# Performance work log

Hardware: AMD Instinct MI355X
Metric: run time of the kernel (lower is better)

Reference implementation:

```python
import jax, jax.numpy as jnp
import numpy as np

B, L, D = 4, 2048, 256
H, HD = 8, 64
MAX_LEN = 2048


def setup_inputs() -> dict:
    key = jax.random.key(0)
    ks = jax.random.split(key, 5)
    x = jax.random.normal(ks[0], (B, L, D), dtype=jnp.float32)
    glorot_q = (2.0 / (D + H * HD)) ** 0.5
    Wq = jax.random.normal(ks[1], (D, H * HD), dtype=jnp.float32) * glorot_q
    Wk = jax.random.normal(ks[2], (D, H * HD), dtype=jnp.float32) * glorot_q
    bq = jnp.zeros((H, 1, 1, HD), dtype=jnp.float32)
    bk = jnp.zeros((H, 1, 1, HD), dtype=jnp.float32)
    prior_mean = jax.random.uniform(ks[3], (H,), dtype=jnp.float32, minval=-1.0, maxval=1.0)
    log_prior_std = jnp.full((H,), np.log(0.4), dtype=jnp.float32)
    return {"x": x, "Wq": Wq, "bq": bq, "Wk": Wk, "bk": bk,
            "prior_mean": prior_mean, "log_prior_std": log_prior_std,
            "max_length": MAX_LEN}


def _gaussian(x, mean, std):
    return 1.0 / std / jnp.sqrt(2.0 * 3.1415926) * jnp.exp(-0.5 * (x - mean) ** 2 / std ** 2)


def reference(x, Wq, bq, Wk, bk, prior_mean, log_prior_std, max_length):
    b, l, d = x.shape
    h, hd = bq.shape[0], bq.shape[-1]
    # normalized signed distance matrix [l, l]
    r = jnp.arange(l, dtype=jnp.float32)
    dist = (r[None, :] - r[:, None]) / float(max_length)
    # projections -> [h, b, l, hd] (split heads along last dim, heads leading)
    q = (x @ Wq).reshape(b, l, h, hd).transpose(2, 0, 1, 3) + bq
    k = (x @ Wk).reshape(b, l, h, hd).transpose(2, 0, 1, 3) + bk
    # gaussian positional prior per head [h, l, l]
    prior = _gaussian(dist[None, :, :], prior_mean[:, None, None],
                      jnp.exp(log_prior_std)[:, None, None])
    # scaled QK^T * prior -> softmax over keys
    scores = jnp.einsum('hbqd,hbkd->hbqk', q, k) * (float(hd) ** -0.5)
    att = jax.nn.softmax(scores * prior[:, None, :, :], axis=-1)
    # distance-weighted reduction instead of V-matmul: [h, b, l] -> [b, l, h]
    distance = jnp.einsum('hbqk,qk->hbq', att, dist)
    return distance.transpose(1, 2, 0)
```

## Files before the change

### kernel.cpp

```cpp
#include <hip/hip_runtime.h>
#include <math.h>


#define B_  4
#define L_  2048
#define D_  256
#define H_  8
#define HD_ 64

typedef unsigned int u32;
typedef unsigned short u16;
typedef short bf16x8 __attribute__((ext_vector_type(8)));
typedef float f32x4  __attribute__((ext_vector_type(4)));

union U16x8 { u16 u[8]; bf16x8 v; uint4 q; };

__device__ __forceinline__ u16 bf16rne(float v) {
    u32 u = __float_as_uint(v);
    return (u16)((u + 0x7fffu + ((u >> 16) & 1u)) >> 16);
}
__device__ __forceinline__ float bf2f(u16 h) { return __uint_as_float(((u32)h) << 16); }

__global__ __launch_bounds__(256, 4) void proj_kernel(
    const float* __restrict__ x,
    const float* __restrict__ Wq, const float* __restrict__ bq,
    const float* __restrict__ Wk, const float* __restrict__ bk,
    u16* __restrict__ Qhi, u16* __restrict__ Qlo,
    u16* __restrict__ Khi, u16* __restrict__ Klo)
{
    __shared__ __align__(16) u16 Bs[2][64][40];

    const int z = blockIdx.z;
    const float* W    = z ? Wk : Wq;
    const float* bias = z ? bk : bq;
    u16* Ohi = z ? Khi : Qhi;
    u16* Olo = z ? Klo : Qlo;

    const int t = threadIdx.x, w = t >> 6, l = t & 63;
    const int kc = l & 15, lhi = l >> 4;
    const int m0 = blockIdx.x * 128 + w * 32;
    const int h  = blockIdx.y;

    const float* xp0 = x + (size_t)(m0 + kc) * D_;
    const float* xp1 = x + (size_t)(m0 + 16 + kc) * D_;

    f32x4 acc[2][4];
    #pragma unroll
    for (int mf = 0; mf < 2; ++mf)
        #pragma unroll
        for (int nf = 0; nf < 4; ++nf) acc[mf][nf] = (f32x4){0.f, 0.f, 0.f, 0.f};

    for (int ks = 0; ks < 8; ++ks) {
        __syncthreads();
        #pragma unroll
        for (int j = 0; j < 2; ++j) {
            const int fid = t + j * 256;
            const int kr = fid >> 4, c4 = fid & 15;
            float4 v = *(const float4*)&W[(size_t)(ks*32 + kr) * 512 + h*64 + c4*4];
            float vv[4] = {v.x, v.y, v.z, v.w};
            #pragma unroll
            for (int e = 0; e < 4; ++e) {
                const int n = c4*4 + e;
                const u16 hi = bf16rne(vv[e]);
                Bs[0][n][kr] = hi;
                Bs[1][n][kr] = bf16rne(vv[e] - bf2f(hi));
            }
        }
        __syncthreads();

        U16x8 ah[2], al[2];
        #pragma unroll
        for (int mf = 0; mf < 2; ++mf) {
            const float* xp = mf ? xp1 : xp0;
            float4 a = *(const float4*)(xp + ks*32 + lhi*8);
            float4 b = *(const float4*)(xp + ks*32 + lhi*8 + 4);
            float vv[8] = {a.x, a.y, a.z, a.w, b.x, b.y, b.z, b.w};
            #pragma unroll
            for (int e = 0; e < 8; ++e) {
                const u16 hi = bf16rne(vv[e]);
                ah[mf].u[e] = hi;
                al[mf].u[e] = bf16rne(vv[e] - bf2f(hi));
            }
        }

        #pragma unroll
        for (int nf = 0; nf < 4; ++nf) {
            const bf16x8 bh = *(const bf16x8*)&Bs[0][nf*16 + kc][lhi*8];
            const bf16x8 bl = *(const bf16x8*)&Bs[1][nf*16 + kc][lhi*8];
            #pragma unroll
            for (int mf = 0; mf < 2; ++mf) {
                acc[mf][nf] = __builtin_amdgcn_mfma_f32_16x16x32_bf16(ah[mf].v, bh, acc[mf][nf], 0, 0, 0);
                acc[mf][nf] = __builtin_amdgcn_mfma_f32_16x16x32_bf16(ah[mf].v, bl, acc[mf][nf], 0, 0, 0);
                acc[mf][nf] = __builtin_amdgcn_mfma_f32_16x16x32_bf16(al[mf].v, bh, acc[mf][nf], 0, 0, 0);
            }
        }
    }

    #pragma unroll
    for (int mf = 0; mf < 2; ++mf)
        #pragma unroll
        for (int nf = 0; nf < 4; ++nf) {
            const float bv = bias[h * 64 + nf*16 + kc];
            #pragma unroll
            for (int r = 0; r < 4; ++r) {
                const float v = acc[mf][nf][r] + bv;
                const u16 hi = bf16rne(v);
                const u16 lo = bf16rne(v - bf2f(hi));
                const int m = m0 + mf*16 + lhi*4 + r;
                const int bb = m >> 11, ll = m & (L_ - 1);
                const size_t o = (((size_t)h * B_ + bb) * L_ + ll) * HD_ + nf*16 + kc;
                Ohi[o] = hi; Olo[o] = lo;
            }
        }
}

__global__ __launch_bounds__(512, 4) void attn_kernel(
    const u16* __restrict__ Qhi, const u16* __restrict__ Qlo,
    const u16* __restrict__ Khi, const u16* __restrict__ Klo,
    const float* __restrict__ prior_mean, const float* __restrict__ log_prior_std,
    const int* __restrict__ max_len, float* __restrict__ out)
{
    __shared__ __align__(16) u16 kls[2][64 * 64];
    __shared__ float2 Ptab[2176];

    const int t = threadIdx.x, w = t >> 6, l = t & 63;
    const int kc = l & 15, lhi = l >> 4;
    const int q0 = blockIdx.x * 128;
    const int hb = blockIdx.y, h = hb >> 2, b = hb & 3;
    const int qw = q0 + w * 16;

    const float iml = 1.0f / (float)(*max_len);
    const float mu  = prior_mean[h];
    const float sg  = __expf(log_prior_std[h]);
    const float isg = 1.0f / sg;
    const float coef = 0.125f / (sg * 2.5066282746310002f) * 1.44269504089f;
    for (int i = t; i < 2175; i += 512) {
        const float dist = (float)(i - q0 - 127) * iml;
        const float tt = (dist - mu) * isg;
        Ptab[i] = make_float2(coef * __expf(-0.5f * tt * tt), dist);
    }

    bf16x8 qh[2], ql2[2];
    #pragma unroll
    for (int dh = 0; dh < 2; ++dh) {
        const size_t qo = ((size_t)hb * L_ + qw + kc) * HD_ + dh*32 + lhi*8;
        qh[dh]  = *(const bf16x8*)&Qhi[qo];
        ql2[dh] = *(const bf16x8*)&Qlo[qo];
    }

    const float2* pbase = &Ptab[lhi*4 + 127 - w*16 - kc];

    const int spl = t >> 8;
    const int srow = (t & 255) >> 2;
    const int sq = t & 3;
    const int sr7 = srow & 7;
    const u16* Kg = (spl ? Klo : Khi) + ((size_t)hb * L_ + srow) * HD_ + sq * 16;
    u16* lds_row = &kls[spl][srow * 64];

    const int sl0 = lhi ^ (l & 7);
    const int sl1 = (4 + lhi) ^ (l & 7);

    float lv = 0.f, wv = 0.f;

    for (int kt = 0; kt < 32; ++kt) {
        __syncthreads();
        {
            const u16* src = Kg + (size_t)kt * 64 * HD_;
            const uint4 g0 = *(const uint4*)src;
            const uint4 g1 = *(const uint4*)(src + 8);
            const int p0 = (sq*2)     ^ sr7;
            const int p1 = (sq*2 + 1) ^ sr7;
            *(uint4*)&lds_row[p0 * 8] = g0;
            *(uint4*)&lds_row[p1 * 8] = g1;
        }
        __syncthreads();

        f32x4 acc[4];
        #pragma unroll
        for (int kf = 0; kf < 4; ++kf) acc[kf] = (f32x4){0.f, 0.f, 0.f, 0.f};

        #pragma unroll
        for (int kf = 0; kf < 4; ++kf) {
            const int rbase = (kf*16 + kc) * 64;
            const bf16x8 ah0 = *(const bf16x8*)&kls[0][rbase + sl0*8];
            const bf16x8 ah1 = *(const bf16x8*)&kls[0][rbase + sl1*8];
            const bf16x8 al0 = *(const bf16x8*)&kls[1][rbase + sl0*8];
            const bf16x8 al1 = *(const bf16x8*)&kls[1][rbase + sl1*8];
            acc[kf] = __builtin_amdgcn_mfma_f32_16x16x32_bf16(ah0, qh[0],  acc[kf], 0, 0, 0);
            acc[kf] = __builtin_amdgcn_mfma_f32_16x16x32_bf16(ah1, qh[1],  acc[kf], 0, 0, 0);
            acc[kf] = __builtin_amdgcn_mfma_f32_16x16x32_bf16(ah0, ql2[0], acc[kf], 0, 0, 0);
            acc[kf] = __builtin_amdgcn_mfma_f32_16x16x32_bf16(ah1, ql2[1], acc[kf], 0, 0, 0);
            acc[kf] = __builtin_amdgcn_mfma_f32_16x16x32_bf16(al0, qh[0],  acc[kf], 0, 0, 0);
            acc[kf] = __builtin_amdgcn_mfma_f32_16x16x32_bf16(al1, qh[1],  acc[kf], 0, 0, 0);
        }

        const float2* pp = pbase + kt * 64;
        #pragma unroll
        for (int kf = 0; kf < 4; ++kf)
            #pragma unroll
            for (int r = 0; r < 4; ++r) {
                const float2 pd = pp[kf*16 + r];
                const float e = exp2f(acc[kf][r] * pd.x);
                lv += e;
                wv = fmaf(e, pd.y, wv);
            }
    }

    lv += __shfl_xor(lv, 16); wv += __shfl_xor(wv, 16);
    lv += __shfl_xor(lv, 32); wv += __shfl_xor(wv, 32);
    if (lhi == 0) {
        const int q = qw + kc;
        out[((size_t)(b * L_ + q)) * H_ + h] = wv / lv;
    }
}

extern "C" void kernel_launch(void* const* d_in, const int* in_sizes, int n_in,
                              void* d_out, int out_size, void* d_ws, size_t ws_size,
                              hipStream_t stream)
{
    const float* x   = (const float*)d_in[0];
    const float* Wq  = (const float*)d_in[1];
    const float* bq  = (const float*)d_in[2];
    const float* Wk  = (const float*)d_in[3];
    const float* bk  = (const float*)d_in[4];
    const float* pm  = (const float*)d_in[5];
    const float* lps = (const float*)d_in[6];
    const int*   mlp = (const int*)d_in[7];
    float* out = (float*)d_out;

    u16* Qhi = (u16*)d_ws;
    u16* Qlo = Qhi + 4194304;
    u16* Khi = Qlo + 4194304;
    u16* Klo = Khi + 4194304;

    proj_kernel<<<dim3(64, 8, 2), 256, 0, stream>>>(x, Wq, bq, Wk, bk, Qhi, Qlo, Khi, Klo);
    attn_kernel<<<dim3(16, 32), 512, 0, stream>>>(Qhi, Qlo, Khi, Klo, pm, lps, mlp, out);
}
```

Before: 163.4 us.

## Restructure attention kernel with double-buffered K tiles, larger query tiles, inline prior

The attention kernel now gives each wave 32 query rows instead of 16, so each K tile in LDS feeds twice as many MFMAs. K tiles are double-buffered with register prefetch so global loads overlap compute, and the grid is remapped to 256 blocks grouped by XCD. The Gaussian prior table in LDS is replaced by inline exp2 of a quadratic, and the distance-weighted sum is factored into a per-tile base plus a column offset. In exchange the kernel uses more registers (launch bounds drop to 2 blocks per CU), does more transcendental work per element, and changes the float summation order.

After: 169.5 us. +3.8%, slower.

```diff
diff --git a/kernel.cpp b/kernel.cpp
--- a/kernel.cpp
+++ b/kernel.cpp
@@ -13,15 +13,19 @@
 typedef short bf16x8 __attribute__((ext_vector_type(8)));
 typedef float f32x4  __attribute__((ext_vector_type(4)));
 
-union U16x8 { u16 u[8]; bf16x8 v; uint4 q; };
-
 __device__ __forceinline__ u16 bf16rne(float v) {
     u32 u = __float_as_uint(v);
     return (u16)((u + 0x7fffu + ((u >> 16) & 1u)) >> 16);
 }
 __device__ __forceinline__ float bf2f(u16 h) { return __uint_as_float(((u32)h) << 16); }
 
-__global__ __launch_bounds__(256, 4) void proj_kernel(
+#if __has_builtin(__builtin_amdgcn_exp2f)
+__device__ __forceinline__ float fast_exp2(float x) { return __builtin_amdgcn_exp2f(x); }
+#else
+__device__ __forceinline__ float fast_exp2(float x) { return exp2f(x); }
+#endif
+
+__global__ __launch_bounds__(256, 4) void projB_kernel(
     const float* __restrict__ x,
     const float* __restrict__ Wq, const float* __restrict__ bq,
     const float* __restrict__ Wk, const float* __restrict__ bk,
@@ -68,7 +72,7 @@
         }
         __syncthreads();
 
-        U16x8 ah[2], al[2];
+        union { u16 u[8]; bf16x8 v; } ah[2], al[2];
         #pragma unroll
         for (int mf = 0; mf < 2; ++mf) {
             const float* xp = mf ? xp1 : xp0;
@@ -114,103 +118,134 @@
         }
 }
 
-__global__ __launch_bounds__(512, 4) void attn_kernel(
+__global__ __launch_bounds__(512, 2) void attn_kernel(
     const u16* __restrict__ Qhi, const u16* __restrict__ Qlo,
     const u16* __restrict__ Khi, const u16* __restrict__ Klo,
     const float* __restrict__ prior_mean, const float* __restrict__ log_prior_std,
     const int* __restrict__ max_len, float* __restrict__ out)
 {
-    __shared__ __align__(16) u16 kls[2][64 * 64];
-    __shared__ float2 Ptab[2176];
+    __shared__ __align__(16) u16 kls[2][2][64 * 64];
 
     const int t = threadIdx.x, w = t >> 6, l = t & 63;
     const int kc = l & 15, lhi = l >> 4;
-    const int q0 = blockIdx.x * 128;
-    const int hb = blockIdx.y, h = hb >> 2, b = hb & 3;
-    const int qw = q0 + w * 16;
+
+    const int p = blockIdx.x;
+    const int xcd = p & 7, s = p >> 3;
+    const int hb = xcd * 4 + (s >> 3);
+    const int q0 = (s & 7) * 256;
+    const int h = hb >> 2, b = hb & 3;
+    const int qw = q0 + w * 32;
 
     const float iml = 1.0f / (float)(*max_len);
     const float mu  = prior_mean[h];
     const float sg  = __expf(log_prior_std[h]);
     const float isg = 1.0f / sg;
-    const float coef = 0.125f / (sg * 2.5066282746310002f) * 1.44269504089f;
-    for (int i = t; i < 2175; i += 512) {
-        const float dist = (float)(i - q0 - 127) * iml;
-        const float tt = (dist - mu) * isg;
-        Ptab[i] = make_float2(coef * __expf(-0.5f * tt * tt), dist);
-    }
-
-    bf16x8 qh[2], ql2[2];
+    const float S2  = 0.84932180f;
+    const float A2  = iml * isg * S2;
+    const float B2  = -mu * isg * S2;
+    const float LC  = __log2f(0.125f * 1.44269504089f / (sg * 2.5066282746310002f));
+
+    bf16x8 qh[2][2], ql2[2][2];
     #pragma unroll
-    for (int dh = 0; dh < 2; ++dh) {
-        const size_t qo = ((size_t)hb * L_ + qw + kc) * HD_ + dh*32 + lhi*8;
-        qh[dh]  = *(const bf16x8*)&Qhi[qo];
-        ql2[dh] = *(const bf16x8*)&Qlo[qo];
-    }
-
-    const float2* pbase = &Ptab[lhi*4 + 127 - w*16 - kc];
+    for (int qf = 0; qf < 2; ++qf)
+        #pragma unroll
+        for (int dh = 0; dh < 2; ++dh) {
+            const size_t qo = ((size_t)hb * L_ + qw + qf*16 + kc) * HD_ + dh*32 + lhi*8;
+            qh[qf][dh]  = *(const bf16x8*)&Qhi[qo];
+            ql2[qf][dh] = *(const bf16x8*)&Qlo[qo];
+        }
+
+    const int d0q0 = lhi*4 - (q0 + w*32 + kc);
+    const int d0q1 = d0q0 - 16;
 
     const int spl = t >> 8;
     const int srow = (t & 255) >> 2;
     const int sq = t & 3;
     const int sr7 = srow & 7;
     const u16* Kg = (spl ? Klo : Khi) + ((size_t)hb * L_ + srow) * HD_ + sq * 16;
-    u16* lds_row = &kls[spl][srow * 64];
-
-    const int sl0 = lhi ^ (l & 7);
-    const int sl1 = (4 + lhi) ^ (l & 7);
-
-    float lv = 0.f, wv = 0.f;
-
-    for (int kt = 0; kt < 32; ++kt) {
-        __syncthreads();
-        {
-            const u16* src = Kg + (size_t)kt * 64 * HD_;
-            const uint4 g0 = *(const uint4*)src;
-            const uint4 g1 = *(const uint4*)(src + 8);
-            const int p0 = (sq*2)     ^ sr7;
-            const int p1 = (sq*2 + 1) ^ sr7;
-            *(uint4*)&lds_row[p0 * 8] = g0;
-            *(uint4*)&lds_row[p1 * 8] = g1;
-        }
-        __syncthreads();
-
-        f32x4 acc[4];
-        #pragma unroll
-        for (int kf = 0; kf < 4; ++kf) acc[kf] = (f32x4){0.f, 0.f, 0.f, 0.f};
-
-        #pragma unroll
-        for (int kf = 0; kf < 4; ++kf) {
-            const int rbase = (kf*16 + kc) * 64;
-            const bf16x8 ah0 = *(const bf16x8*)&kls[0][rbase + sl0*8];
-            const bf16x8 ah1 = *(const bf16x8*)&kls[0][rbase + sl1*8];
-            const bf16x8 al0 = *(const bf16x8*)&kls[1][rbase + sl0*8];
-            const bf16x8 al1 = *(const bf16x8*)&kls[1][rbase + sl1*8];
-            acc[kf] = __builtin_amdgcn_mfma_f32_16x16x32_bf16(ah0, qh[0],  acc[kf], 0, 0, 0);
-            acc[kf] = __builtin_amdgcn_mfma_f32_16x16x32_bf16(ah1, qh[1],  acc[kf], 0, 0, 0);
-            acc[kf] = __builtin_amdgcn_mfma_f32_16x16x32_bf16(ah0, ql2[0], acc[kf], 0, 0, 0);
-            acc[kf] = __builtin_amdgcn_mfma_f32_16x16x32_bf16(ah1, ql2[1], acc[kf], 0, 0, 0);
-            acc[kf] = __builtin_amdgcn_mfma_f32_16x16x32_bf16(al0, qh[0],  acc[kf], 0, 0, 0);
-            acc[kf] = __builtin_amdgcn_mfma_f32_16x16x32_bf16(al1, qh[1],  acc[kf], 0, 0, 0);
-        }
-
-        const float2* pp = pbase + kt * 64;
-        #pragma unroll
-        for (int kf = 0; kf < 4; ++kf)
-            #pragma unroll
-            for (int r = 0; r < 4; ++r) {
-                const float2 pd = pp[kf*16 + r];
-                const float e = exp2f(acc[kf][r] * pd.x);
-                lv += e;
-                wv = fmaf(e, pd.y, wv);
-            }
+    const int p0 = ((sq*2)     ^ sr7) * 8;
+    const int p1 = ((sq*2 + 1) ^ sr7) * 8;
+    u16* wdst0 = &kls[0][spl][srow * 64];
+    u16* wdst1 = &kls[1][spl][srow * 64];
+
+    const int sl0 = (lhi ^ (kc & 7)) * 8;
+    const int sl1 = ((4 + lhi) ^ (kc & 7)) * 8;
+
+    float lv0 = 0.f, wv0 = 0.f, lv1 = 0.f, wv1 = 0.f;
+
+    uint4 ra0, ra1, rb0, rb1;
+    ra0 = *(const uint4*)Kg; ra1 = *(const uint4*)(Kg + 8);
+    *(uint4*)&wdst0[p0] = ra0; *(uint4*)&wdst0[p1] = ra1;
+    ra0 = *(const uint4*)(Kg + 4096); ra1 = *(const uint4*)(Kg + 4096 + 8);
+    __syncthreads();
+
+#define LOADT(RX0, RX1, TI) { const u16* src_ = Kg + (size_t)(TI) * 4096; \
+    RX0 = *(const uint4*)src_; RX1 = *(const uint4*)(src_ + 8); }
+#define WRT(DST, RX0, RX1) { *(uint4*)&DST[p0] = RX0; *(uint4*)&DST[p1] = RX1; }
+#define CTILE(TI, BS) { \
+    const u16* bh_ = &kls[BS][0][0]; const u16* bl_ = &kls[BS][1][0]; \
+    f32x4 acc[4][2]; \
+    _Pragma("unroll") for (int kf = 0; kf < 4; ++kf) { \
+        acc[kf][0] = (f32x4){0.f,0.f,0.f,0.f}; acc[kf][1] = (f32x4){0.f,0.f,0.f,0.f}; } \
+    __builtin_amdgcn_s_setprio(1); \
+    _Pragma("unroll") for (int kf = 0; kf < 4; ++kf) { \
+        const int rb_ = (kf*16 + kc) * 64; \
+        const bf16x8 ah0 = *(const bf16x8*)&bh_[rb_ + sl0]; \
+        const bf16x8 ah1 = *(const bf16x8*)&bh_[rb_ + sl1]; \
+        const bf16x8 al0 = *(const bf16x8*)&bl_[rb_ + sl0]; \
+        const bf16x8 al1 = *(const bf16x8*)&bl_[rb_ + sl1]; \
+        _Pragma("unroll") for (int qf = 0; qf < 2; ++qf) { \
+            acc[kf][qf] = __builtin_amdgcn_mfma_f32_16x16x32_bf16(ah0, qh[qf][0],  acc[kf][qf], 0, 0, 0); \
+            acc[kf][qf] = __builtin_amdgcn_mfma_f32_16x16x32_bf16(ah1, qh[qf][1],  acc[kf][qf], 0, 0, 0); \
+            acc[kf][qf] = __builtin_amdgcn_mfma_f32_16x16x32_bf16(ah0, ql2[qf][0], acc[kf][qf], 0, 0, 0); \
+            acc[kf][qf] = __builtin_amdgcn_mfma_f32_16x16x32_bf16(ah1, ql2[qf][1], acc[kf][qf], 0, 0, 0); \
+            acc[kf][qf] = __builtin_amdgcn_mfma_f32_16x16x32_bf16(al0, qh[qf][0],  acc[kf][qf], 0, 0, 0); \
+            acc[kf][qf] = __builtin_amdgcn_mfma_f32_16x16x32_bf16(al1, qh[qf][1],  acc[kf][qf], 0, 0, 0); \
+        } \
+    } \
+    __builtin_amdgcn_s_setprio(0); \
+    _Pragma("unroll") for (int qf = 0; qf < 2; ++qf) { \
+        const float dbf = (float)((TI)*64 + (qf ? d0q1 : d0q0)); \
+        const float t2b = fmaf(dbf, A2, B2); \
+        float S0 = 0.f, S1 = 0.f; \
+        _Pragma("unroll") for (int kf = 0; kf < 4; ++kf) \
+            _Pragma("unroll") for (int r = 0; r < 4; ++r) { \
+                const int cc = kf*16 + r; \
+                const float t2c = fmaf((float)cc, A2, t2b); \
+                const float pr  = fast_exp2(fmaf(-t2c, t2c, LC)); \
+                const float e   = fast_exp2(acc[kf][qf][r] * pr); \
+                S0 += e; if (cc) S1 = fmaf(e, (float)cc, S1); \
+            } \
+        if (qf == 0) { lv0 += S0; wv0 = fmaf(dbf, S0, wv0 + S1); } \
+        else         { lv1 += S0; wv1 = fmaf(dbf, S0, wv1 + S1); } \
+    } \
+}
+
+    for (int kt = 0; kt < 32; kt += 2) {
+        if (kt + 2 < 32) LOADT(rb0, rb1, kt + 2);
+        WRT(wdst1, ra0, ra1);
+        CTILE(kt, 0);
+        __syncthreads();
+        if (kt + 3 < 32) LOADT(ra0, ra1, kt + 3);
+        if (kt + 2 < 32) WRT(wdst0, rb0, rb1);
+        CTILE(kt + 1, 1);
+        __syncthreads();
     }
-
-    lv += __shfl_xor(lv, 16); wv += __shfl_xor(wv, 16);
-    lv += __shfl_xor(lv, 32); wv += __shfl_xor(wv, 32);
+#undef LOADT
+#undef WRT
+#undef CTILE
+
+    lv0 += __shfl_xor(lv0, 16); wv0 += __shfl_xor(wv0, 16);
+    lv0 += __shfl_xor(lv0, 32); wv0 += __shfl_xor(wv0, 32);
+    lv1 += __shfl_xor(lv1, 16); wv1 += __shfl_xor(wv1, 16);
+    lv1 += __shfl_xor(lv1, 32); wv1 += __shfl_xor(wv1, 32);
+
     if (lhi == 0) {
         const int q = qw + kc;
-        out[((size_t)(b * L_ + q)) * H_ + h] = wv / lv;
+        out[((size_t)(b * L_ + q)) * H_ + h] = (wv0 * iml) / lv0;
+    } else if (lhi == 1) {
+        const int q = qw + 16 + kc;
+        out[((size_t)(b * L_ + q)) * H_ + h] = (wv1 * iml) / lv1;
     }
 }
 
@@ -233,6 +268,7 @@
     u16* Khi = Qlo + 4194304;
     u16* Klo = Khi + 4194304;
 
-    proj_kernel<<<dim3(64, 8, 2), 256, 0, stream>>>(x, Wq, bq, Wk, bk, Qhi, Qlo, Khi, Klo);
-    attn_kernel<<<dim3(16, 32), 512, 0, stream>>>(Qhi, Qlo, Khi, Klo, pm, lps, mlp, out);
-}
+    projB_kernel<<<dim3(64, 8, 2), 256, 0, stream>>>(x, Wq, bq, Wk, bk,
+                                                     Qhi, Qlo, Khi, Klo);
+    attn_kernel<<<dim3(256), 512, 0, stream>>>(Qhi, Qlo, Khi, Klo, pm, lps, mlp, out);
+}
```
